# Kernel optimization log

Measured on AMD Instinct MI355X. Metric: run time of the kernel, lower is better.

## Reference

```python
import jax, jax.numpy as jnp
import numpy as np

B, S, D, H = 2, 2048, 2048, 16
DH = D // H            # attention_inner_dim = 128
FF = 4 * D             # feedforward_inner_dim = 8192
EPS = 1e-6


def layernorm(x, gamma, beta):
    m = jnp.mean(x, axis=-1, keepdims=True)
    v = jnp.mean((x - m) ** 2, axis=-1, keepdims=True)
    return gamma * (x - m) / jnp.sqrt(v + EPS) + beta


def rotate_half(x):
    # source rotate_half: swap halves without negation
    h = x.shape[-1] // 2
    return jnp.concatenate([x[..., h:], x[..., :h]], axis=-1)


def setup_inputs() -> dict:
    key = jax.random.key(0)
    ks = jax.random.split(key, 8)
    d = {}
    d['x'] = jax.random.normal(ks[0], (B, S, D), dtype=jnp.float32) * 0.02
    d['W_fused'] = jax.random.normal(ks[1], (D, 3 * D + FF), dtype=jnp.float32) * (D ** -0.5)
    d['b_fused'] = jnp.zeros((3 * D + FF,), dtype=jnp.float32)
    d['W_attn'] = jax.random.normal(ks[2], (D, D), dtype=jnp.float32) * (D ** -0.5)
    d['b_attn'] = jnp.zeros((D,), dtype=jnp.float32)
    d['W_ff'] = jax.random.normal(ks[3], (FF, D), dtype=jnp.float32) * (FF ** -0.5)
    d['b_ff'] = jnp.zeros((D,), dtype=jnp.float32)
    d['gamma1'] = jnp.ones((FF,), dtype=jnp.float32)
    d['beta1'] = jnp.zeros((FF,), dtype=jnp.float32)
    d['gamma2'] = jnp.ones((D,), dtype=jnp.float32)
    d['beta2'] = jnp.zeros((D,), dtype=jnp.float32)
    # learned rotary table, shape [n_positions>=S, head_dim], std = head_dim**-0.5
    d['rope_w'] = jax.random.normal(ks[4], (S, DH), dtype=jnp.float32) * (DH ** -0.5)
    return d


def reference(x, W_fused, b_fused, W_attn, b_attn, W_ff, b_ff,
              gamma1, beta1, gamma2, beta2, rope_w):
    # fused QKV + FFN projection (single GEMM)
    fused = x @ W_fused + b_fused                       # [B,S,3D+FF]
    q, k, v, ff = jnp.split(fused, [D, 2 * D, 3 * D], axis=-1)
    q = q.reshape(B, S, H, DH).transpose(0, 2, 1, 3)    # [B,H,S,DH]
    k = k.reshape(B, S, H, DH).transpose(0, 2, 1, 3)
    v = v.reshape(B, S, H, DH).transpose(0, 2, 1, 3)

    # inline rotary embedding from learned per-position table
    pe = rope_w[:S]                                     # [S,DH]
    cos, sin = jnp.cos(pe), jnp.sin(pe)

    def rope(t):
        return t * cos + rotate_half(t) * sin

    q = rope(q) * (DH ** -0.5)
    k = rope(k)

    # manual causal attention
    sim = jnp.einsum('bhqd,bhkd->bhqk', q, k)           # [B,H,S,S]
    causal = jnp.tril(jnp.ones((S, S), dtype=bool))
    sim = jnp.where(causal, sim, jnp.finfo(sim.dtype).min)
    attn_w = jax.nn.softmax(sim, axis=-1)
    o = jnp.einsum('bhqk,bhkd->bhqd', attn_w, v)        # [B,H,S,DH]
    o = o.transpose(0, 2, 1, 3).reshape(B, S, D)
    attn = o @ W_attn + b_attn                          # [B,S,D]

    # parallel feedforward branch: norm -> relu -> proj -> silu (SwiGLU in src is x*sigmoid(x))
    h = jax.nn.relu(layernorm(ff, gamma1, beta1))
    ffo = h @ W_ff + b_ff
    ffo = ffo * jax.nn.sigmoid(ffo)

    return layernorm(attn + ffo, gamma2, beta2)
```

## Files before the change

kernel.cpp:

```cpp
#include <hip/hip_runtime.h>
#include <hip/hip_bf16.h>
#include <cmath>

#define BB 2
#define SS 2048
#define DD 2048
#define HHN 16
#define DHH 128
#define FFF 8192
#define NFF (3*DD+FFF)
#define MR (BB*SS)
#define LNEPS 1e-6f

typedef __hip_bfloat16 bf16;
using bf16x8 = __attribute__((ext_vector_type(8))) __bf16;
using f32x4  = __attribute__((ext_vector_type(4))) float;

__device__ __forceinline__ void async_copy16(const bf16* g, bf16* l) {
  __builtin_amdgcn_global_load_lds(
      (const __attribute__((address_space(1))) void*)g,
      (__attribute__((address_space(3))) void*)l, 16, 0, 0);
}

__global__ __launch_bounds__(256) void k_convert(const float* __restrict__ in,
                                                 bf16* __restrict__ out, int n4) {
  int i = blockIdx.x * 256 + threadIdx.x;
  if (i >= n4) return;
  float4 v = ((const float4*)in)[i];
  out[4*i+0] = __float2bfloat16(v.x);
  out[4*i+1] = __float2bfloat16(v.y);
  out[4*i+2] = __float2bfloat16(v.z);
  out[4*i+3] = __float2bfloat16(v.w);
}

__global__ __launch_bounds__(256) void k_transpose(const float* __restrict__ in,
                                                   bf16* __restrict__ out, int R, int C) {
  __shared__ float tile[32][33];
  int c0 = blockIdx.x * 32, r0 = blockIdx.y * 32;
  int tx = threadIdx.x, ty = threadIdx.y;
  #pragma unroll
  for (int i = 0; i < 32; i += 8)
    tile[ty + i][tx] = in[(size_t)(r0 + ty + i) * C + (c0 + tx)];
  __syncthreads();
  #pragma unroll
  for (int i = 0; i < 32; i += 8)
    out[(size_t)(c0 + ty + i) * R + (r0 + tx)] = __float2bfloat16(tile[tx][ty + i]);
}

__global__ __launch_bounds__(256) void k_gemm_bt(const bf16* __restrict__ A,
                                                 const bf16* __restrict__ BT,
                                                 const float* __restrict__ bias,
                                                 void* __restrict__ Cout,
                                                 const float* __restrict__ addin,
                                                 int M, int N, int K, int mode) {
  __shared__ __align__(16) bf16 As[128 * 32];
  __shared__ __align__(16) bf16 Bs[128 * 32];
  int tid = threadIdx.x;
  int w = tid >> 6, l = tid & 63;
  int wm = w >> 1, wn = w & 1;
  int l15 = l & 15, g = l >> 4;
  int sr4 = l >> 2, sc4 = (l & 3) * 8;
  int m0 = blockIdx.y * 128, n0 = blockIdx.x * 128;

  f32x4 acc[4][4];
  #pragma unroll
  for (int i = 0; i < 4; i++)
    #pragma unroll
    for (int j = 0; j < 4; j++)
      acc[i][j] = f32x4{0.f, 0.f, 0.f, 0.f};

  for (int k0 = 0; k0 < K; k0 += 32) {
    __syncthreads();
    #pragma unroll
    for (int i = 0; i < 2; i++) {
      int r = (w * 2 + i) * 16 + sr4;
      async_copy16(A + (size_t)(m0 + r) * K + k0 + sc4, &As[r * 32 + sc4]);
      async_copy16(BT + (size_t)(n0 + r) * K + k0 + sc4, &Bs[r * 32 + sc4]);
    }
    __syncthreads();

    bf16x8 af[4], bf_[4];
    #pragma unroll
    for (int i = 0; i < 4; i++)
      af[i] = *reinterpret_cast<const bf16x8*>(&As[(wm * 64 + i * 16 + l15) * 32 + g * 8]);
    #pragma unroll
    for (int j = 0; j < 4; j++)
      bf_[j] = *reinterpret_cast<const bf16x8*>(&Bs[(wn * 64 + j * 16 + l15) * 32 + g * 8]);
    #pragma unroll
    for (int i = 0; i < 4; i++)
      #pragma unroll
      for (int j = 0; j < 4; j++)
        acc[i][j] = __builtin_amdgcn_mfma_f32_16x16x32_bf16(af[i], bf_[j], acc[i][j], 0, 0, 0);
  }

  float* Cf = (float*)Cout;
  bf16* Cb = (bf16*)Cout;
  #pragma unroll
  for (int i = 0; i < 4; i++) {
    #pragma unroll
    for (int j = 0; j < 4; j++) {
      int mbase = m0 + wm * 64 + i * 16 + g * 4;
      int nn = n0 + wn * 64 + j * 16 + l15;
      float bv = bias[nn];
      #pragma unroll
      for (int rr = 0; rr < 4; rr++) {
        size_t idx = (size_t)(mbase + rr) * N + nn;
        float v = acc[i][j][rr] + bv;
        if (mode == 0) {
          Cf[idx] = v;
        } else if (mode == 1) {
          Cb[idx] = __float2bfloat16(v);
        } else {
          float sig = 1.f / (1.f + expf(-v));
          Cf[idx] = addin[idx] + v * sig;
        }
      }
    }
  }
}

__global__ __launch_bounds__(256) void k_rope(bf16* __restrict__ fused,
                                              const float* __restrict__ rope_w) {
  int row = blockIdx.x;
  int s = row & (SS - 1);
  const float* rw = rope_w + (size_t)s * DHH;
  const float scale = 0.08838834764831845f;
  for (int idx = threadIdx.x; idx < HHN * 64; idx += 256) {
    int h = idx >> 6, d = idx & 63;
    float c1 = cosf(rw[d]),      s1 = sinf(rw[d]);
    float c2 = cosf(rw[d + 64]), s2 = sinf(rw[d + 64]);
    bf16* q = fused + (size_t)row * NFF + h * DHH;
    bf16* k = q + DD;
    float q0 = __bfloat162float(q[d]), q1 = __bfloat162float(q[d + 64]);
    q[d]      = __float2bfloat16((q0 * c1 + q1 * s1) * scale);
    q[d + 64] = __float2bfloat16((q1 * c2 + q0 * s2) * scale);
    float k0 = __bfloat162float(k[d]), k1 = __bfloat162float(k[d + 64]);
    k[d]      = __float2bfloat16(k0 * c1 + k1 * s1);
    k[d + 64] = __float2bfloat16(k1 * c2 + k0 * s2);
  }
}

__global__ __launch_bounds__(256) void k_flash(const bf16* __restrict__ fused,
                                               bf16* __restrict__ obuf) {
  constexpr int LDP = 72;
  __shared__ __align__(16) bf16 Qs[64 * LDP];
  __shared__ __align__(16) bf16 Ks[64 * LDP];
  __shared__ __align__(16) bf16 Vt[128 * LDP];
  __shared__ __align__(16) bf16 Ps[64 * LDP];
  int qb = blockIdx.x, bh = blockIdx.y;
  int b = bh >> 4, h = bh & 15;
  int tid = threadIdx.x;
  int wave = tid >> 6, lane = tid & 63;
  int l15 = lane & 15, g = lane >> 4;

  const bf16* qbase = fused + (size_t)(b * SS + qb * 64) * NFF + h * DHH;
  const bf16* kbase = fused + (size_t)(b * SS) * NFF + DD + h * DHH;
  const bf16* vbase = kbase + DD;

  {
    int r = tid >> 4, dc = tid & 15;
    #pragma unroll
    for (int i = 0; i < 4; i++) {
      int row = r + 16 * i;
      *reinterpret_cast<bf16x8*>(&Qs[row * LDP + dc * 8]) =
          *reinterpret_cast<const bf16x8*>(qbase + (size_t)row * NFF + dc * 8);
    }
  }
  __syncthreads();
  bf16x8 qf[4];
  #pragma unroll
  for (int ks = 0; ks < 4; ks++)
    qf[ks] = *reinterpret_cast<const bf16x8*>(&Qs[(wave * 16 + l15) * LDP + ks * 32 + g * 8]);

  f32x4 o[8];
  #pragma unroll
  for (int nt = 0; nt < 8; nt++) o[nt] = f32x4{0.f, 0.f, 0.f, 0.f};
  float m_i[4], l_i[4];
  #pragma unroll
  for (int r = 0; r < 4; r++) { m_i[r] = -1e30f; l_i[r] = 0.f; }
  int qrow_base = qb * 64 + wave * 16 + g * 4;

  for (int kt = 0; kt <= qb; kt++) {
    __syncthreads();
    {
      int r = tid >> 4, dc = tid & 15;
      #pragma unroll
      for (int i = 0; i < 4; i++) {
        int key = r + 16 * i;
        *reinterpret_cast<bf16x8*>(&Ks[key * LDP + dc * 8]) =
            *reinterpret_cast<const bf16x8*>(kbase + (size_t)(kt * 64 + key) * NFF + dc * 8);
      }
      int vkey = tid & 63, dc0 = tid >> 6;
      #pragma unroll
      for (int i = 0; i < 4; i++) {
        int dchunk = dc0 + i * 4;
        bf16x8 vv = *reinterpret_cast<const bf16x8*>(
            vbase + (size_t)(kt * 64 + vkey) * NFF + dchunk * 8);
        #pragma unroll
        for (int j = 0; j < 8; j++)
          *(__bf16*)&Vt[(dchunk * 8 + j) * LDP + vkey] = vv[j];
      }
    }
    __syncthreads();

    f32x4 s[4];
    #pragma unroll
    for (int nt = 0; nt < 4; nt++) {
      s[nt] = f32x4{0.f, 0.f, 0.f, 0.f};
      #pragma unroll
      for (int ks = 0; ks < 4; ks++) {
        bf16x8 bfrag = *reinterpret_cast<const bf16x8*>(
            &Ks[(nt * 16 + l15) * LDP + ks * 32 + g * 8]);
        s[nt] = __builtin_amdgcn_mfma_f32_16x16x32_bf16(qf[ks], bfrag, s[nt], 0, 0, 0);
      }
    }
    #pragma unroll
    for (int nt = 0; nt < 4; nt++) {
      int kk = kt * 64 + nt * 16 + l15;
      #pragma unroll
      for (int r = 0; r < 4; r++)
        if (kk > qrow_base + r) s[nt][r] = -1e30f;
    }
    float alpha[4];
    #pragma unroll
    for (int r = 0; r < 4; r++) {
      float mx = fmaxf(fmaxf(s[0][r], s[1][r]), fmaxf(s[2][r], s[3][r]));
      mx = fmaxf(mx, __shfl_xor(mx, 1));
      mx = fmaxf(mx, __shfl_xor(mx, 2));
      mx = fmaxf(mx, __shfl_xor(mx, 4));
      mx = fmaxf(mx, __shfl_xor(mx, 8));
      float mnew = fmaxf(m_i[r], mx);
      alpha[r] = __expf(m_i[r] - mnew);
      m_i[r] = mnew;
      float ls = 0.f;
      #pragma unroll
      for (int nt = 0; nt < 4; nt++) {
        float p = __expf(s[nt][r] - mnew);
        s[nt][r] = p;
        ls += p;
      }
      ls += __shfl_xor(ls, 1);
      ls += __shfl_xor(ls, 2);
      ls += __shfl_xor(ls, 4);
      ls += __shfl_xor(ls, 8);
      l_i[r] = l_i[r] * alpha[r] + ls;
    }
    #pragma unroll
    for (int nt = 0; nt < 4; nt++)
      #pragma unroll
      for (int r = 0; r < 4; r++)
        *(__bf16*)&Ps[(wave * 16 + g * 4 + r) * LDP + nt * 16 + l15] = (__bf16)s[nt][r];
    #pragma unroll
    for (int nt = 0; nt < 8; nt++)
      #pragma unroll
      for (int r = 0; r < 4; r++) o[nt][r] *= alpha[r];
    bf16x8 pf[2];
    #pragma unroll
    for (int ks = 0; ks < 2; ks++)
      pf[ks] = *reinterpret_cast<const bf16x8*>(
          &Ps[(wave * 16 + l15) * LDP + ks * 32 + g * 8]);
    #pragma unroll
    for (int nt = 0; nt < 8; nt++)
      #pragma unroll
      for (int ks = 0; ks < 2; ks++) {
        bf16x8 bfrag = *reinterpret_cast<const bf16x8*>(
            &Vt[(nt * 16 + l15) * LDP + ks * 32 + g * 8]);
        o[nt] = __builtin_amdgcn_mfma_f32_16x16x32_bf16(pf[ks], bfrag, o[nt], 0, 0, 0);
      }
  }

  float inv[4];
  #pragma unroll
  for (int r = 0; r < 4; r++) inv[r] = 1.f / l_i[r];
  #pragma unroll
  for (int nt = 0; nt < 8; nt++)
    #pragma unroll
    for (int r = 0; r < 4; r++) {
      size_t row = (size_t)(b * SS + qrow_base + r);
      obuf[row * DD + h * DHH + nt * 16 + l15] = __float2bfloat16(o[nt][r] * inv[r]);
    }
}

__global__ __launch_bounds__(256) void k_ln1_relu(const bf16* __restrict__ fused,
                                                  const float* __restrict__ gamma,
                                                  const float* __restrict__ beta,
                                                  bf16* __restrict__ h) {
  int row = blockIdx.x;
  const bf16* xr = fused + (size_t)row * NFF + 3 * DD;
  int tid = threadIdx.x;
  float s = 0.f, ss = 0.f;
  for (int i = tid; i < FFF; i += 256) {
    float v = __bfloat162float(xr[i]);
    s += v; ss += v * v;
  }
  #pragma unroll
  for (int off = 32; off > 0; off >>= 1) { s += __shfl_down(s, off); ss += __shfl_down(ss, off); }
  __shared__ float red[8];
  int wave = tid >> 6, lane = tid & 63;
  if (lane == 0) { red[wave] = s; red[4 + wave] = ss; }
  __syncthreads();
  if (tid == 0) {
    float S0 = red[0] + red[1] + red[2] + red[3];
    float SQ = red[4] + red[5] + red[6] + red[7];
    float m = S0 / FFF;
    float var = SQ / FFF - m * m;
    red[0] = m;
    red[1] = 1.f / sqrtf(var + LNEPS);
  }
  __syncthreads();
  float m = red[0], inv = red[1];
  for (int i = tid; i < FFF; i += 256) {
    float v = __bfloat162float(xr[i]);
    float y = gamma[i] * (v - m) * inv + beta[i];
    h[(size_t)row * FFF + i] = __float2bfloat16(fmaxf(y, 0.f));
  }
}

__global__ __launch_bounds__(256) void k_ln2(const float* __restrict__ yin,
                                             const float* __restrict__ gamma,
                                             const float* __restrict__ beta,
                                             float* __restrict__ out) {
  int row = blockIdx.x;
  const float* xr = yin + (size_t)row * DD;
  int tid = threadIdx.x;
  float s = 0.f, ss = 0.f;
  for (int i = tid; i < DD; i += 256) {
    float v = xr[i];
    s += v; ss += v * v;
  }
  #pragma unroll
  for (int off = 32; off > 0; off >>= 1) { s += __shfl_down(s, off); ss += __shfl_down(ss, off); }
  __shared__ float red[8];
  int wave = tid >> 6, lane = tid & 63;
  if (lane == 0) { red[wave] = s; red[4 + wave] = ss; }
  __syncthreads();
  if (tid == 0) {
    float S0 = red[0] + red[1] + red[2] + red[3];
    float SQ = red[4] + red[5] + red[6] + red[7];
    float m = S0 / DD;
    float var = SQ / DD - m * m;
    red[0] = m;
    red[1] = 1.f / sqrtf(var + LNEPS);
  }
  __syncthreads();
  float m = red[0], inv = red[1];
  for (int i = tid; i < DD; i += 256) {
    float v = xr[i];
    out[(size_t)row * DD + i] = gamma[i] * (v - m) * inv + beta[i];
  }
}

extern "C" void kernel_launch(void* const* d_in, const int* in_sizes, int n_in,
                              void* d_out, int out_size, void* d_ws, size_t ws_size,
                              hipStream_t stream) {
  const float* x       = (const float*)d_in[0];
  const float* W_fused = (const float*)d_in[1];
  const float* b_fused = (const float*)d_in[2];
  const float* W_attn  = (const float*)d_in[3];
  const float* b_attn  = (const float*)d_in[4];
  const float* W_ff    = (const float*)d_in[5];
  const float* b_ff    = (const float*)d_in[6];
  const float* gamma1  = (const float*)d_in[7];
  const float* beta1   = (const float*)d_in[8];
  const float* gamma2  = (const float*)d_in[9];
  const float* beta2   = (const float*)d_in[10];
  const float* rope_w  = (const float*)d_in[11];

  char* ws = (char*)d_ws;
  size_t off = 0;
  auto alloc = [&](size_t bytes) -> void* {
    void* p = ws + off;
    off += (bytes + 255) & ~(size_t)255;
    return p;
  };
  bf16* fused = (bf16*)alloc((size_t)MR * NFF * 2);
  bf16* xb    = (bf16*)alloc((size_t)MR * DD * 2);
  bf16* WfT   = (bf16*)alloc((size_t)NFF * DD * 2);
  bf16* WaT   = (bf16*)alloc((size_t)DD * DD * 2);
  bf16* WffT  = (bf16*)alloc((size_t)DD * FFF * 2);
  bf16* hbuf  = (bf16*)alloc((size_t)MR * FFF * 2);
  bf16* obuf  = (bf16*)alloc((size_t)MR * DD * 2);
  float* ybuf = (float*)alloc((size_t)MR * DD * 4);
  if (off > ws_size) return;

  k_convert<<<(MR * DD / 4 + 255) / 256, 256, 0, stream>>>(x, xb, MR * DD / 4);
  k_transpose<<<dim3(NFF / 32, DD / 32), dim3(32, 8), 0, stream>>>(W_fused, WfT, DD, NFF);
  k_transpose<<<dim3(DD / 32, DD / 32), dim3(32, 8), 0, stream>>>(W_attn, WaT, DD, DD);
  k_transpose<<<dim3(DD / 32, FFF / 32), dim3(32, 8), 0, stream>>>(W_ff, WffT, FFF, DD);
  k_gemm_bt<<<dim3(NFF / 128, MR / 128), 256, 0, stream>>>(xb, WfT, b_fused, fused, nullptr,
                                                           MR, NFF, DD, 1);
  k_rope<<<MR, 256, 0, stream>>>(fused, rope_w);
  k_flash<<<dim3(SS / 64, BB * HHN), 256, 0, stream>>>(fused, obuf);
  k_gemm_bt<<<dim3(DD / 128, MR / 128), 256, 0, stream>>>(obuf, WaT, b_attn, ybuf, nullptr,
                                                          MR, DD, DD, 0);
  k_ln1_relu<<<MR, 256, 0, stream>>>(fused, gamma1, beta1, hbuf);
  k_gemm_bt<<<dim3(DD / 128, MR / 128), 256, 0, stream>>>(hbuf, WffT, b_ff, ybuf, ybuf,
                                                          MR, DD, FFF, 2);
  k_ln2<<<MR, 256, 0, stream>>>(ybuf, gamma2, beta2, (float*)d_out);
}
```

Before: 1.305 ms.

## Pre-transpose V, async-load flash tiles, precompute sincos, vectorize LN/rope, swizzle GEMM grid

```diff
diff --git a/kernel.cpp b/kernel.cpp
--- a/kernel.cpp
+++ b/kernel.cpp
@@ -47,6 +47,22 @@
     out[(size_t)(c0 + ty + i) * R + (r0 + tx)] = __float2bfloat16(tile[tx][ty + i]);
 }
 
+__global__ void k_vtrans(const bf16* __restrict__ fused, bf16* __restrict__ vT) {
+  __shared__ bf16 tile[32][33];
+  int s0 = blockIdx.x * 32, d0 = blockIdx.y * 32, bh = blockIdx.z;
+  int b = bh >> 4, h = bh & 15;
+  int tx = threadIdx.x, ty = threadIdx.y;
+  const bf16* src = fused + (size_t)(b * SS) * NFF + 2 * DD + h * DHH;
+  #pragma unroll
+  for (int i = 0; i < 32; i += 8)
+    tile[ty + i][tx] = src[(size_t)(s0 + ty + i) * NFF + d0 + tx];
+  __syncthreads();
+  bf16* dst = vT + ((size_t)bh * DHH) * SS;
+  #pragma unroll
+  for (int i = 0; i < 32; i += 8)
+    dst[(size_t)(d0 + ty + i) * SS + s0 + tx] = tile[tx][ty + i];
+}
+
 __global__ __launch_bounds__(256) void k_gemm_bt(const bf16* __restrict__ A,
                                                  const bf16* __restrict__ BT,
                                                  const float* __restrict__ bias,
@@ -55,12 +71,17 @@
                                                  int M, int N, int K, int mode) {
   __shared__ __align__(16) bf16 As[128 * 32];
   __shared__ __align__(16) bf16 Bs[128 * 32];
+  int NBm = M >> 7;
+  constexpr int PW = 16;
+  int bid = blockIdx.x;
+  int pid = bid / (PW * NBm), rem = bid % (PW * NBm);
+  int by = rem / PW, bx = pid * PW + rem % PW;
   int tid = threadIdx.x;
   int w = tid >> 6, l = tid & 63;
   int wm = w >> 1, wn = w & 1;
   int l15 = l & 15, g = l >> 4;
   int sr4 = l >> 2, sc4 = (l & 3) * 8;
-  int m0 = blockIdx.y * 128, n0 = blockIdx.x * 128;
+  int m0 = by * 128, n0 = bx * 128;
 
   f32x4 acc[4][4];
   #pragma unroll
@@ -119,58 +140,70 @@
   }
 }
 
+__global__ __launch_bounds__(256) void k_sincos(const float* __restrict__ rope_w,
+                                                float2* __restrict__ tab) {
+  int i = blockIdx.x * 256 + threadIdx.x;
+  if (i >= SS * DHH) return;
+  float v = rope_w[i];
+  tab[i] = make_float2(cosf(v), sinf(v));
+}
+
 __global__ __launch_bounds__(256) void k_rope(bf16* __restrict__ fused,
-                                              const float* __restrict__ rope_w) {
+                                              const float2* __restrict__ tab) {
   int row = blockIdx.x;
   int s = row & (SS - 1);
-  const float* rw = rope_w + (size_t)s * DHH;
+  const float2* tr = tab + (size_t)s * DHH;
+  int tid = threadIdx.x;
+  int isK = tid >> 7, ch = tid & 127;
+  int h = ch >> 3, c0 = (ch & 7) * 8;
   const float scale = 0.08838834764831845f;
-  for (int idx = threadIdx.x; idx < HHN * 64; idx += 256) {
-    int h = idx >> 6, d = idx & 63;
-    float c1 = cosf(rw[d]),      s1 = sinf(rw[d]);
-    float c2 = cosf(rw[d + 64]), s2 = sinf(rw[d + 64]);
-    bf16* q = fused + (size_t)row * NFF + h * DHH;
-    bf16* k = q + DD;
-    float q0 = __bfloat162float(q[d]), q1 = __bfloat162float(q[d + 64]);
-    q[d]      = __float2bfloat16((q0 * c1 + q1 * s1) * scale);
-    q[d + 64] = __float2bfloat16((q1 * c2 + q0 * s2) * scale);
-    float k0 = __bfloat162float(k[d]), k1 = __bfloat162float(k[d + 64]);
-    k[d]      = __float2bfloat16(k0 * c1 + k1 * s1);
-    k[d + 64] = __float2bfloat16(k1 * c2 + k0 * s2);
-  }
+  bf16* base = fused + (size_t)row * NFF + isK * DD + h * DHH;
+  bf16x8 lo = *reinterpret_cast<const bf16x8*>(base + c0);
+  bf16x8 hi = *reinterpret_cast<const bf16x8*>(base + c0 + 64);
+  bf16x8 olo, ohi;
+  #pragma unroll
+  for (int t = 0; t < 8; t++) {
+    int d = c0 + t;
+    float2 cl = tr[d], chh = tr[d + 64];
+    float x0 = (float)lo[t], x1 = (float)hi[t];
+    float r0 = x0 * cl.x + x1 * cl.y;
+    float r1 = x1 * chh.x + x0 * chh.y;
+    if (!isK) { r0 *= scale; r1 *= scale; }
+    olo[t] = (__bf16)r0;
+    ohi[t] = (__bf16)r1;
+  }
+  *reinterpret_cast<bf16x8*>(base + c0) = olo;
+  *reinterpret_cast<bf16x8*>(base + c0 + 64) = ohi;
 }
 
 __global__ __launch_bounds__(256) void k_flash(const bf16* __restrict__ fused,
+                                               const bf16* __restrict__ vT,
                                                bf16* __restrict__ obuf) {
-  constexpr int LDP = 72;
-  __shared__ __align__(16) bf16 Qs[64 * LDP];
-  __shared__ __align__(16) bf16 Ks[64 * LDP];
-  __shared__ __align__(16) bf16 Vt[128 * LDP];
-  __shared__ __align__(16) bf16 Ps[64 * LDP];
+  __shared__ __align__(16) bf16 smem[20480];
+  bf16* Ks = smem;
+  bf16* Vt = smem + 8192;
+  bf16* Ps = smem + 16384;
+  bf16* Qs = smem;
+
   int qb = blockIdx.x, bh = blockIdx.y;
   int b = bh >> 4, h = bh & 15;
   int tid = threadIdx.x;
-  int wave = tid >> 6, lane = tid & 63;
-  int l15 = lane & 15, g = lane >> 4;
+  int w = tid >> 6, l = tid & 63;
+  int l15 = l & 15, g = l >> 4;
 
   const bf16* qbase = fused + (size_t)(b * SS + qb * 64) * NFF + h * DHH;
   const bf16* kbase = fused + (size_t)(b * SS) * NFF + DD + h * DHH;
-  const bf16* vbase = kbase + DD;
-
-  {
-    int r = tid >> 4, dc = tid & 15;
-    #pragma unroll
-    for (int i = 0; i < 4; i++) {
-      int row = r + 16 * i;
-      *reinterpret_cast<bf16x8*>(&Qs[row * LDP + dc * 8]) =
-          *reinterpret_cast<const bf16x8*>(qbase + (size_t)row * NFF + dc * 8);
-    }
-  }
+  const bf16* vtb = vT + (size_t)bh * DHH * SS;
+
+  #pragma unroll
+  for (int ks = 0; ks < 4; ks++)
+    async_copy16(qbase + (size_t)(w * 16 + (l >> 2)) * NFF + ks * 32 + (l & 3) * 8,
+                 &Qs[ks * 2048 + w * 512 + l * 8]);
   __syncthreads();
   bf16x8 qf[4];
   #pragma unroll
   for (int ks = 0; ks < 4; ks++)
-    qf[ks] = *reinterpret_cast<const bf16x8*>(&Qs[(wave * 16 + l15) * LDP + ks * 32 + g * 8]);
+    qf[ks] = *reinterpret_cast<const bf16x8*>(&Qs[ks * 2048 + (w * 16 + l15) * 32 + g * 8]);
 
   f32x4 o[8];
   #pragma unroll
@@ -178,29 +211,20 @@
   float m_i[4], l_i[4];
   #pragma unroll
   for (int r = 0; r < 4; r++) { m_i[r] = -1e30f; l_i[r] = 0.f; }
-  int qrow_base = qb * 64 + wave * 16 + g * 4;
+  int qrow_base = qb * 64 + w * 16 + g * 4;
 
   for (int kt = 0; kt <= qb; kt++) {
     __syncthreads();
-    {
-      int r = tid >> 4, dc = tid & 15;
-      #pragma unroll
-      for (int i = 0; i < 4; i++) {
-        int key = r + 16 * i;
-        *reinterpret_cast<bf16x8*>(&Ks[key * LDP + dc * 8]) =
-            *reinterpret_cast<const bf16x8*>(kbase + (size_t)(kt * 64 + key) * NFF + dc * 8);
-      }
-      int vkey = tid & 63, dc0 = tid >> 6;
-      #pragma unroll
-      for (int i = 0; i < 4; i++) {
-        int dchunk = dc0 + i * 4;
-        bf16x8 vv = *reinterpret_cast<const bf16x8*>(
-            vbase + (size_t)(kt * 64 + vkey) * NFF + dchunk * 8);
-        #pragma unroll
-        for (int j = 0; j < 8; j++)
-          *(__bf16*)&Vt[(dchunk * 8 + j) * LDP + vkey] = vv[j];
-      }
-    }
+    #pragma unroll
+    for (int ks = 0; ks < 4; ks++)
+      async_copy16(kbase + (size_t)(kt * 64 + w * 16 + (l >> 2)) * NFF + ks * 32 + (l & 3) * 8,
+                   &Ks[ks * 2048 + w * 512 + l * 8]);
+    #pragma unroll
+    for (int j = 0; j < 2; j++)
+      #pragma unroll
+      for (int kc = 0; kc < 2; kc++)
+        async_copy16(vtb + (size_t)(j * 64 + w * 16 + (l >> 2)) * SS + kt * 64 + kc * 32 + (l & 3) * 8,
+                     &Vt[kc * 4096 + j * 2048 + w * 512 + l * 8]);
     __syncthreads();
 
     f32x4 s[4];
@@ -210,7 +234,7 @@
       #pragma unroll
       for (int ks = 0; ks < 4; ks++) {
         bf16x8 bfrag = *reinterpret_cast<const bf16x8*>(
-            &Ks[(nt * 16 + l15) * LDP + ks * 32 + g * 8]);
+            &Ks[ks * 2048 + (nt * 16 + l15) * 32 + g * 8]);
         s[nt] = __builtin_amdgcn_mfma_f32_16x16x32_bf16(qf[ks], bfrag, s[nt], 0, 0, 0);
       }
     }
@@ -246,10 +270,13 @@
       l_i[r] = l_i[r] * alpha[r] + ls;
     }
     #pragma unroll
-    for (int nt = 0; nt < 4; nt++)
+    for (int nt = 0; nt < 4; nt++) {
+      int kk = nt * 16 + l15;
       #pragma unroll
       for (int r = 0; r < 4; r++)
-        *(__bf16*)&Ps[(wave * 16 + g * 4 + r) * LDP + nt * 16 + l15] = (__bf16)s[nt][r];
+        *(__bf16*)&Ps[(kk >> 5) * 2048 + (w * 16 + g * 4 + r) * 32 + (kk & 31)] =
+            (__bf16)s[nt][r];
+    }
     #pragma unroll
     for (int nt = 0; nt < 8; nt++)
       #pragma unroll
@@ -258,13 +285,13 @@
     #pragma unroll
     for (int ks = 0; ks < 2; ks++)
       pf[ks] = *reinterpret_cast<const bf16x8*>(
-          &Ps[(wave * 16 + l15) * LDP + ks * 32 + g * 8]);
+          &Ps[ks * 2048 + (w * 16 + l15) * 32 + g * 8]);
     #pragma unroll
     for (int nt = 0; nt < 8; nt++)
       #pragma unroll
       for (int ks = 0; ks < 2; ks++) {
         bf16x8 bfrag = *reinterpret_cast<const bf16x8*>(
-            &Vt[(nt * 16 + l15) * LDP + ks * 32 + g * 8]);
+            &Vt[ks * 4096 + (nt * 16 + l15) * 32 + g * 8]);
         o[nt] = __builtin_amdgcn_mfma_f32_16x16x32_bf16(pf[ks], bfrag, o[nt], 0, 0, 0);
       }
   }
@@ -288,10 +315,16 @@
   int row = blockIdx.x;
   const bf16* xr = fused + (size_t)row * NFF + 3 * DD;
   int tid = threadIdx.x;
+  bf16x8 v8[4];
   float s = 0.f, ss = 0.f;
-  for (int i = tid; i < FFF; i += 256) {
-    float v = __bfloat162float(xr[i]);
-    s += v; ss += v * v;
+  #pragma unroll
+  for (int k = 0; k < 4; k++) {
+    v8[k] = *reinterpret_cast<const bf16x8*>(xr + (tid + k * 256) * 8);
+    #pragma unroll
+    for (int t = 0; t < 8; t++) {
+      float v = (float)v8[k][t];
+      s += v; ss += v * v;
+    }
   }
   #pragma unroll
   for (int off = 32; off > 0; off >>= 1) { s += __shfl_down(s, off); ss += __shfl_down(ss, off); }
@@ -309,10 +342,18 @@
   }
   __syncthreads();
   float m = red[0], inv = red[1];
-  for (int i = tid; i < FFF; i += 256) {
-    float v = __bfloat162float(xr[i]);
-    float y = gamma[i] * (v - m) * inv + beta[i];
-    h[(size_t)row * FFF + i] = __float2bfloat16(fmaxf(y, 0.f));
+  bf16* hr = h + (size_t)row * FFF;
+  #pragma unroll
+  for (int k = 0; k < 4; k++) {
+    bf16x8 o8;
+    int base = (tid + k * 256) * 8;
+    #pragma unroll
+    for (int t = 0; t < 8; t++) {
+      float v = (float)v8[k][t];
+      float y = gamma[base + t] * (v - m) * inv + beta[base + t];
+      o8[t] = (__bf16)fmaxf(y, 0.f);
+    }
+    *reinterpret_cast<bf16x8*>(hr + base) = o8;
   }
 }
 
@@ -321,12 +362,15 @@
                                              const float* __restrict__ beta,
                                              float* __restrict__ out) {
   int row = blockIdx.x;
-  const float* xr = yin + (size_t)row * DD;
+  const float4* xr = (const float4*)(yin + (size_t)row * DD);
   int tid = threadIdx.x;
+  float4 v4[2];
   float s = 0.f, ss = 0.f;
-  for (int i = tid; i < DD; i += 256) {
-    float v = xr[i];
-    s += v; ss += v * v;
+  #pragma unroll
+  for (int k = 0; k < 2; k++) {
+    v4[k] = xr[tid + k * 256];
+    s += v4[k].x + v4[k].y + v4[k].z + v4[k].w;
+    ss += v4[k].x * v4[k].x + v4[k].y * v4[k].y + v4[k].z * v4[k].z + v4[k].w * v4[k].w;
   }
   #pragma unroll
   for (int off = 32; off > 0; off >>= 1) { s += __shfl_down(s, off); ss += __shfl_down(ss, off); }
@@ -344,9 +388,16 @@
   }
   __syncthreads();
   float m = red[0], inv = red[1];
-  for (int i = tid; i < DD; i += 256) {
-    float v = xr[i];
-    out[(size_t)row * DD + i] = gamma[i] * (v - m) * inv + beta[i];
+  float4* orow = (float4*)(out + (size_t)row * DD);
+  #pragma unroll
+  for (int k = 0; k < 2; k++) {
+    int base = (tid + k * 256) * 4;
+    float4 r;
+    r.x = gamma[base + 0] * (v4[k].x - m) * inv + beta[base + 0];
+    r.y = gamma[base + 1] * (v4[k].y - m) * inv + beta[base + 1];
+    r.z = gamma[base + 2] * (v4[k].z - m) * inv + beta[base + 2];
+    r.w = gamma[base + 3] * (v4[k].w - m) * inv + beta[base + 3];
+    orow[tid + k * 256] = r;
   }
 }
 
@@ -382,19 +433,23 @@
   bf16* obuf  = (bf16*)alloc((size_t)MR * DD * 2);
   float* ybuf = (float*)alloc((size_t)MR * DD * 4);
   if (off > ws_size) return;
+  bf16* vT = xb;
+  float2* tab = (float2*)ybuf;
 
   k_convert<<<(MR * DD / 4 + 255) / 256, 256, 0, stream>>>(x, xb, MR * DD / 4);
+  k_sincos<<<(SS * DHH + 255) / 256, 256, 0, stream>>>(rope_w, tab);
   k_transpose<<<dim3(NFF / 32, DD / 32), dim3(32, 8), 0, stream>>>(W_fused, WfT, DD, NFF);
   k_transpose<<<dim3(DD / 32, DD / 32), dim3(32, 8), 0, stream>>>(W_attn, WaT, DD, DD);
   k_transpose<<<dim3(DD / 32, FFF / 32), dim3(32, 8), 0, stream>>>(W_ff, WffT, FFF, DD);
-  k_gemm_bt<<<dim3(NFF / 128, MR / 128), 256, 0, stream>>>(xb, WfT, b_fused, fused, nullptr,
-                                                           MR, NFF, DD, 1);
-  k_rope<<<MR, 256, 0, stream>>>(fused, rope_w);
-  k_flash<<<dim3(SS / 64, BB * HHN), 256, 0, stream>>>(fused, obuf);
-  k_gemm_bt<<<dim3(DD / 128, MR / 128), 256, 0, stream>>>(obuf, WaT, b_attn, ybuf, nullptr,
-                                                          MR, DD, DD, 0);
+  k_gemm_bt<<<(NFF / 128) * (MR / 128), 256, 0, stream>>>(xb, WfT, b_fused, fused, nullptr,
+                                                          MR, NFF, DD, 1);
+  k_rope<<<MR, 256, 0, stream>>>(fused, tab);
+  k_vtrans<<<dim3(SS / 32, DHH / 32, BB * HHN), dim3(32, 8), 0, stream>>>(fused, vT);
+  k_flash<<<dim3(SS / 64, BB * HHN), 256, 0, stream>>>(fused, vT, obuf);
+  k_gemm_bt<<<(DD / 128) * (MR / 128), 256, 0, stream>>>(obuf, WaT, b_attn, ybuf, nullptr,
+                                                         MR, DD, DD, 0);
   k_ln1_relu<<<MR, 256, 0, stream>>>(fused, gamma1, beta1, hbuf);
-  k_gemm_bt<<<dim3(DD / 128, MR / 128), 256, 0, stream>>>(hbuf, WffT, b_ff, ybuf, ybuf,
-                                                          MR, DD, FFF, 2);
+  k_gemm_bt<<<(DD / 128) * (MR / 128), 256, 0, stream>>>(hbuf, WffT, b_ff, ybuf, ybuf,
+                                                         MR, DD, FFF, 2);
   k_ln2<<<MR, 256, 0, stream>>>(ybuf, gamma2, beta2, (float*)d_out);
 }
```

Measured after the change: 1.176 ms. 1.11x faster.
